# Optimization experiments

Hardware: AMD Instinct MI355X
Metric: run time of the kernel (lower is better)

The kernel has to match this reference:

```python
import jax, jax.numpy as jnp
import numpy as np

B, N, H, HD = 2, 2048, 16, 64
F = H * HD  # feats = 1024
SQRT_D = float(F) ** 0.5  # module uses sqrt(feats), not sqrt(head_dim)
EPS = 1e-5


def layernorm(x, g, b):
    # LayerNorm over last dim (head_dim), shared gamma/beta across heads
    m = jnp.mean(x, axis=-1, keepdims=True)
    v = jnp.mean(jnp.square(x - m), axis=-1, keepdims=True)
    return (x - m) / jnp.sqrt(v + EPS) * g + b


def setup_inputs() -> dict:
    key = jax.random.key(0)
    ks = jax.random.split(key, 14)
    s = 0.02
    return {
        "x": jax.random.normal(ks[0], (B, N, F), dtype=jnp.float32),
        "ln1_g": jnp.ones((HD,), jnp.float32),
        "ln1_b": jnp.zeros((HD,), jnp.float32),
        "ln2_g": jnp.ones((HD,), jnp.float32),
        "ln2_b": jnp.zeros((HD,), jnp.float32),
        # stacked per-head weights: [H, in, out]
        "wq": jax.random.normal(ks[1], (H, HD, HD), jnp.float32) * s,
        "bq": jnp.zeros((H, HD), jnp.float32),
        "wk": jax.random.normal(ks[2], (H, HD, HD), jnp.float32) * s,
        "bk": jnp.zeros((H, HD), jnp.float32),
        "wv": jax.random.normal(ks[3], (H, HD, HD), jnp.float32) * s,
        "bv": jnp.zeros((H, HD), jnp.float32),
        "wo": jax.random.normal(ks[4], (H, HD, HD), jnp.float32) * s,
        "bo": jnp.zeros((H, HD), jnp.float32),
        "w1": jax.random.normal(ks[5], (H, HD, 4 * HD), jnp.float32) * s,
        "b1": jnp.zeros((H, 4 * HD), jnp.float32),
        "w2": jax.random.normal(ks[6], (H, 4 * HD, HD), jnp.float32) * s,
        "b2": jnp.zeros((H, HD), jnp.float32),
        # Method 0 merge Linear(feats, feats): y = x @ wm + bm
        "wm": jax.random.normal(ks[7], (F, F), jnp.float32) * s,
        "bm": jnp.zeros((F,), jnp.float32),
    }


def reference(x, ln1_g, ln1_b, ln2_g, ln2_b, wq, bq, wk, bk, wv, bv, wo, bo,
              w1, b1, w2, b2, wm, bm):
    b, n, f = x.shape
    x4 = x.reshape(b, n, H, HD)  # [b, n, h, hd]

    # --- Multi-head self attention (per-head linears batched over h) ---
    h1 = layernorm(x4, ln1_g, ln1_b)
    q = jnp.einsum("bnhf,hfg->bnhg", h1, wq) + bq
    k = jnp.einsum("bnhf,hfg->bnhg", h1, wk) + bk
    v = jnp.einsum("bnhf,hfg->bnhg", h1, wv) + bv
    qh = jnp.swapaxes(q, 1, 2)  # [b, h, n, hd]
    kh = jnp.swapaxes(k, 1, 2)
    vh = jnp.swapaxes(v, 1, 2)
    score = jax.nn.softmax(jnp.einsum("bhif,bhjf->bhij", qh, kh) / SQRT_D, axis=-1)
    attn = jnp.einsum("bhij,bhjf->bihf", score, vh)  # [b, n, h, hd]
    attn = jnp.einsum("bnhf,hfg->bnhg", attn, wo) + bo
    out = attn + x4

    # --- Per-head FFN (GELU after BOTH linears, as in source; dropout=0) ---
    h2 = layernorm(out, ln2_g, ln2_b)
    t = jax.nn.gelu(jnp.einsum("bnhf,hfg->bnhg", h2, w1) + b1, approximate=False)
    t = jax.nn.gelu(jnp.einsum("bnhg,hgf->bnhf", t, w2) + b2, approximate=False)
    out = t + out

    # --- Method 0 merge ---
    out = out.reshape(b, n, f)
    out = out @ wm + bm
    return out
```

## Files before the change

kernel.cpp:

```cpp
#include <hip/hip_runtime.h>
#include <hip/hip_bf16.h>
#include <math.h>

#define TOKS 4096
#define NSEQ 2048
#define NH 16
#define DH 64
#define FD 1024

typedef __bf16 bf16_t;
typedef bf16_t bf16x4 __attribute__((ext_vector_type(4)));
typedef bf16_t bf16x8 __attribute__((ext_vector_type(8)));
typedef float f32x4 __attribute__((ext_vector_type(4)));

#define GLL16(gsrc, ldst)                                                        \
    __builtin_amdgcn_global_load_lds(                                            \
        (const __attribute__((address_space(1))) void*)(const void*)(gsrc),      \
        (__attribute__((address_space(3))) void*)(void*)(ldst), 16, 0, 0)

__device__ __forceinline__ float geluf(float x) {
    return 0.5f * x * (1.0f + erff(x * 0.70710678118654752f));
}

__device__ __forceinline__ int lds_sw(int row, int d) {
    return row * 64 + ((((d >> 3) ^ (row & 7)) & 7) << 3) + (d & 7);
}

__device__ __forceinline__ int vperm(int j) {
    return (j & 32) | ((j & 12) << 1) | ((j & 16) >> 2) | (j & 3);
}

__global__ __launch_bounds__(256) void k_prep(
    const float* __restrict__ wm, const float* __restrict__ w1, const float* __restrict__ w2,
    const float* __restrict__ wq, const float* __restrict__ wk,
    const float* __restrict__ wv, const float* __restrict__ wo,
    bf16_t* __restrict__ wt, bf16_t* __restrict__ w1t, bf16_t* __restrict__ w2t,
    bf16_t* __restrict__ wqt, bf16_t* __restrict__ wkt,
    bf16_t* __restrict__ wvt, bf16_t* __restrict__ wot)
{
    __shared__ bf16_t t[64 * 65];
    const int b = blockIdx.x;
    const int tid = threadIdx.x;
    if (b < 256) {
        const int k0 = (b & 15) * 64, n0 = (b >> 4) * 64;
        #pragma unroll
        for (int it = 0; it < 16; it++) {
            int idx = it * 256 + tid;
            int kk = idx >> 6, nn = idx & 63;
            t[nn * 65 + kk] = (bf16_t)wm[(size_t)(k0 + kk) * FD + n0 + nn];
        }
        __syncthreads();
        #pragma unroll
        for (int it = 0; it < 16; it++) {
            int idx = it * 256 + tid;
            int nn = idx >> 6, kk = idx & 63;
            wt[(size_t)(n0 + nn) * FD + k0 + kk] = t[nn * 65 + kk];
        }
    } else if (b < 320) {
        const int lb = b - 256;
        const int h = lb >> 2, n0 = (lb & 3) * 64;
        const float* src = w1 + (size_t)h * 64 * 256;
        #pragma unroll
        for (int it = 0; it < 16; it++) {
            int idx = it * 256 + tid;
            int kk = idx >> 6, nn = idx & 63;
            t[nn * 65 + kk] = (bf16_t)src[kk * 256 + n0 + nn];
        }
        __syncthreads();
        bf16_t* dst = w1t + (size_t)h * 16384;
        #pragma unroll
        for (int it = 0; it < 16; it++) {
            int idx = it * 256 + tid;
            int nn = idx >> 6, kk = idx & 63;
            int row = n0 + nn;
            dst[row * 64 + ((((kk >> 3) ^ (row & 7)) & 7) << 3) + (kk & 7)] = t[nn * 65 + kk];
        }
    } else if (b < 384) {
        const int lb = b - 320;
        const int h = lb >> 2, k0 = (lb & 3) * 64;
        const float* src = w2 + (size_t)h * 256 * 64;
        #pragma unroll
        for (int it = 0; it < 16; it++) {
            int idx = it * 256 + tid;
            int kk = idx >> 6, nn = idx & 63;
            t[nn * 65 + kk] = (bf16_t)src[(k0 + kk) * 64 + nn];
        }
        __syncthreads();
        bf16_t* dst = w2t + (size_t)h * 16384;
        #pragma unroll
        for (int it = 0; it < 16; it++) {
            int idx = it * 256 + tid;
            int nn = idx >> 6, kk = idx & 63;
            int c = k0 + vperm(kk);
            int chunk = c >> 3;
            int chunkp = (chunk & 24) | ((chunk ^ nn) & 7);
            dst[nn * 256 + (chunkp << 3) + (c & 7)] = t[nn * 65 + kk];
        }
    } else {
        const int h = b - 384;
        const float* srcs[4] = {wq + h * 4096, wk + h * 4096, wv + h * 4096, wo + h * 4096};
        bf16_t* dsts[4] = {wqt + h * 4096, wkt + h * 4096, wvt + h * 4096, wot + h * 4096};
        #pragma unroll
        for (int m = 0; m < 4; m++) {
            __syncthreads();
            #pragma unroll
            for (int it = 0; it < 16; it++) {
                int idx = it * 256 + tid;
                int ff = idx >> 6, gg = idx & 63;
                t[gg * 65 + ff] = (bf16_t)srcs[m][ff * 64 + gg];
            }
            __syncthreads();
            #pragma unroll
            for (int it = 0; it < 16; it++) {
                int idx = it * 256 + tid;
                int gg = idx >> 6, ff = idx & 63;
                if (m == 3)
                    dsts[m][gg * 64 + ((((ff >> 3) ^ (gg & 7)) & 7) << 3) + (ff & 7)] =
                        t[gg * 65 + ff];
                else
                    dsts[m][gg * 64 + ff] = t[gg * 65 + ff];
            }
        }
    }
}

__global__ __launch_bounds__(256) void k_ln1_qkv(
    const float* __restrict__ x, const float* __restrict__ g1, const float* __restrict__ be1,
    const bf16_t* __restrict__ wqt, const float* __restrict__ bq,
    const bf16_t* __restrict__ wkt, const float* __restrict__ bk,
    const bf16_t* __restrict__ wvt, const float* __restrict__ bv,
    bf16_t* __restrict__ q, bf16_t* __restrict__ k, bf16_t* __restrict__ vt)
{
    __shared__ __align__(16) bf16_t h1s[64 * 64];
    __shared__ __align__(16) bf16_t vts[64 * 72];
    const int h  = blockIdx.y;
    const int t0 = blockIdx.x * 64;
    const int tid = threadIdx.x;

    {
        const int i = tid >> 2, s = tid & 3;
        const float* xr = x + (size_t)(t0 + i) * FD + h * DH + s * 16;
        float vals[16];
        #pragma unroll
        for (int r = 0; r < 4; r++) {
            float4 tmp = *(const float4*)(xr + r * 4);
            vals[r*4+0]=tmp.x; vals[r*4+1]=tmp.y; vals[r*4+2]=tmp.z; vals[r*4+3]=tmp.w;
        }
        float sm = 0.f;
        #pragma unroll
        for (int r = 0; r < 16; r++) sm += vals[r];
        sm += __shfl_xor(sm, 1); sm += __shfl_xor(sm, 2);
        const float mean = sm * (1.0f / 64.0f);
        float vr = 0.f;
        #pragma unroll
        for (int r = 0; r < 16; r++) { float d = vals[r] - mean; vr += d * d; }
        vr += __shfl_xor(vr, 1); vr += __shfl_xor(vr, 2);
        const float rstd = rsqrtf(vr * (1.0f / 64.0f) + 1e-5f);
        bf16x8 o0, o1;
        #pragma unroll
        for (int r = 0; r < 8; r++) {
            int d0 = s * 16 + r, d1 = s * 16 + 8 + r;
            o0[r] = (bf16_t)((vals[r]     - mean) * rstd * g1[d0] + be1[d0]);
            o1[r] = (bf16_t)((vals[8 + r] - mean) * rstd * g1[d1] + be1[d1]);
        }
        *(bf16x8*)&h1s[i * 64 + (((s * 2 + 0) ^ (i & 7)) << 3)] = o0;
        *(bf16x8*)&h1s[i * 64 + (((s * 2 + 1) ^ (i & 7)) << 3)] = o1;
    }
    __syncthreads();

    const int wid = tid >> 6, lane = tid & 63;
    const int g = lane >> 4, c0 = lane & 15;
    const int arow = wid * 16 + c0;

    bf16x8 af0 = *(const bf16x8*)&h1s[arow * 64 + (((g    ) ^ (arow & 7)) << 3)];
    bf16x8 af1 = *(const bf16x8*)&h1s[arow * 64 + (((4 + g) ^ (arow & 7)) << 3)];

    const bf16_t* wqh = wqt + h * 4096;
    const bf16_t* wkh = wkt + h * 4096;
    const bf16_t* wvh = wvt + h * 4096;
    f32x4 aq[4], ak[4], av[4];
    #pragma unroll
    for (int ni = 0; ni < 4; ni++) {
        aq[ni] = (f32x4){0.f, 0.f, 0.f, 0.f};
        ak[ni] = (f32x4){0.f, 0.f, 0.f, 0.f};
        av[ni] = (f32x4){0.f, 0.f, 0.f, 0.f};
    }
    #pragma unroll
    for (int ni = 0; ni < 4; ni++) {
        const int col = ni * 16 + c0;
        bf16x8 b0, b1;
        b0 = *(const bf16x8*)(wqh + col * 64 + g * 8);
        b1 = *(const bf16x8*)(wqh + col * 64 + g * 8 + 32);
        aq[ni] = __builtin_amdgcn_mfma_f32_16x16x32_bf16(af0, b0, aq[ni], 0, 0, 0);
        aq[ni] = __builtin_amdgcn_mfma_f32_16x16x32_bf16(af1, b1, aq[ni], 0, 0, 0);
        b0 = *(const bf16x8*)(wkh + col * 64 + g * 8);
        b1 = *(const bf16x8*)(wkh + col * 64 + g * 8 + 32);
        ak[ni] = __builtin_amdgcn_mfma_f32_16x16x32_bf16(af0, b0, ak[ni], 0, 0, 0);
        ak[ni] = __builtin_amdgcn_mfma_f32_16x16x32_bf16(af1, b1, ak[ni], 0, 0, 0);
        b0 = *(const bf16x8*)(wvh + col * 64 + g * 8);
        b1 = *(const bf16x8*)(wvh + col * 64 + g * 8 + 32);
        av[ni] = __builtin_amdgcn_mfma_f32_16x16x32_bf16(af0, b0, av[ni], 0, 0, 0);
        av[ni] = __builtin_amdgcn_mfma_f32_16x16x32_bf16(af1, b1, av[ni], 0, 0, 0);
    }

    const int rowb = wid * 16 + g * 4;
    const int b = t0 >> 11, n0 = t0 & (NSEQ - 1);
    const size_t qkbase = ((size_t)(b * NH + h) * NSEQ + n0) * DH;

    #pragma unroll
    for (int ni = 0; ni < 4; ni++) {
        const int col = ni * 16 + c0;
        const float bb = bv[h * 64 + col];
        #pragma unroll
        for (int r = 0; r < 4; r++) {
            int i = rowb + r;
            vts[col * 72 + vperm(i)] = (bf16_t)(av[ni][r] + bb);
        }
    }
    __syncthreads();

    #pragma unroll
    for (int ni = 0; ni < 4; ni++) {
        const int col = ni * 16 + c0;
        const float bb = bq[h * 64 + col];
        #pragma unroll
        for (int r = 0; r < 4; r++)
            h1s[lds_sw(rowb + r, col)] = (bf16_t)((aq[ni][r] + bb) * 0.045084220f);
    }
    __syncthreads();
    {
        const int row = tid >> 2, cp = (tid & 3) * 2;
        *(bf16x8*)(q + qkbase + row * DH + cp * 8) =
            *(const bf16x8*)&h1s[row * 64 + ((cp ^ (row & 7)) << 3)];
        *(bf16x8*)(q + qkbase + row * DH + (cp + 1) * 8) =
            *(const bf16x8*)&h1s[row * 64 + (((cp + 1) ^ (row & 7)) << 3)];
        const int d = tid >> 2, c16 = tid & 3;
        size_t vbase = ((size_t)(b * NH + h) * DH + d) * NSEQ + n0 + c16 * 16;
        *(bf16x8*)(vt + vbase)     = *(const bf16x8*)&vts[d * 72 + c16 * 16];
        *(bf16x8*)(vt + vbase + 8) = *(const bf16x8*)&vts[d * 72 + c16 * 16 + 8];
    }
    __syncthreads();

    #pragma unroll
    for (int ni = 0; ni < 4; ni++) {
        const int col = ni * 16 + c0;
        const float bb = bk[h * 64 + col];
        #pragma unroll
        for (int r = 0; r < 4; r++)
            h1s[lds_sw(rowb + r, col)] = (bf16_t)(ak[ni][r] + bb);
    }
    __syncthreads();
    {
        const int row = tid >> 2, cp = (tid & 3) * 2;
        *(bf16x8*)(k + qkbase + row * DH + cp * 8) =
            *(const bf16x8*)&h1s[row * 64 + ((cp ^ (row & 7)) << 3)];
        *(bf16x8*)(k + qkbase + row * DH + (cp + 1) * 8) =
            *(const bf16x8*)&h1s[row * 64 + (((cp + 1) ^ (row & 7)) << 3)];
    }
}

__global__ __launch_bounds__(256, 4) void k_attn(
    const bf16_t* __restrict__ qg, const bf16_t* __restrict__ kg,
    const bf16_t* __restrict__ vt, bf16_t* __restrict__ attnb)
{
    __shared__ __align__(16) bf16_t Ks[2][4096];
    __shared__ __align__(16) bf16_t Vs[2][4096];

    const int bx = blockIdx.x;
    const int bh = ((bx & 7) << 2) | ((bx >> 3) & 3);
    const int qb = blockIdx.y;
    const int tid = threadIdx.x;
    const int wid = tid >> 6, lane = tid & 63;
    const int g = lane >> 4, c0 = lane & 15;
    const int prow = wid * 16 + c0;

    bf16x8 aqf[2];
    {
        const int qrow = qb * 64 + prow;
        const bf16_t* qp = qg + ((size_t)bh * NSEQ + qrow) * DH + g * 8;
        aqf[0] = *(const bf16x8*)qp;
        aqf[1] = *(const bf16x8*)(qp + 32);
    }
    bf16x8 ones;
    #pragma unroll
    for (int e = 0; e < 8; e++) ones[e] = (bf16_t)1.0f;

    int soff[4][2];
    #pragma unroll
    for (int cb = 0; cb < 4; cb++)
        #pragma unroll
        for (int kb = 0; kb < 2; kb++) {
            int row = cb * 16 + c0;
            soff[cb][kb] = row * 64 + (((g + (kb << 2)) ^ (row & 7)) << 3);
        }

    const bf16_t* kbase = kg + (size_t)bh * NSEQ * DH;
    const bf16_t* vbase = vt + (size_t)bh * DH * NSEQ;
    const int gA = wid * 2, gB = gA + 1;
    const int lcA = gA * 64 + lane, lcB = gB * 64 + lane;
    const int rowA = lcA >> 3, ccA = (lcA & 7) ^ (rowA & 7);
    const int rowB = lcB >> 3, ccB = (lcB & 7) ^ (rowB & 7);
    const bf16_t* kpA = kbase + rowA * DH + ccA * 8;
    const bf16_t* kpB = kbase + rowB * DH + ccB * 8;
    const bf16_t* vpA = vbase + (size_t)rowA * NSEQ + ccA * 8;
    const bf16_t* vpB = vbase + (size_t)rowB * NSEQ + ccB * 8;

    GLL16(kpA, (char*)&Ks[0][0] + (gA << 10));
    GLL16(kpB, (char*)&Ks[0][0] + (gB << 10));
    GLL16(vpA, (char*)&Vs[0][0] + (gA << 10));
    GLL16(vpB, (char*)&Vs[0][0] + (gB << 10));
    kpA += 64 * DH; kpB += 64 * DH; vpA += 64; vpB += 64;

    f32x4 O[4];
    #pragma unroll
    for (int cb = 0; cb < 4; cb++) O[cb] = (f32x4){0.f, 0.f, 0.f, 0.f};
    f32x4 l_acc = (f32x4){0.f, 0.f, 0.f, 0.f};

    auto tile = [&](const bf16_t* Kc, const bf16_t* Vc,
                    bf16_t* Kn, bf16_t* Vn, bool pref) {
        __syncthreads();
        if (pref) {
            GLL16(kpA, (char*)Kn + (gA << 10));
            GLL16(kpB, (char*)Kn + (gB << 10));
            GLL16(vpA, (char*)Vn + (gA << 10));
            GLL16(vpB, (char*)Vn + (gB << 10));
            kpA += 64 * DH; kpB += 64 * DH; vpA += 64; vpB += 64;
        }

        f32x4 S[4];
        #pragma unroll
        for (int cb = 0; cb < 4; cb++) {
            f32x4 acc = (f32x4){0.f, 0.f, 0.f, 0.f};
            acc = __builtin_amdgcn_mfma_f32_16x16x32_bf16(
                *(const bf16x8*)&Kc[soff[cb][0]], aqf[0], acc, 0, 0, 0);
            acc = __builtin_amdgcn_mfma_f32_16x16x32_bf16(
                *(const bf16x8*)&Kc[soff[cb][1]], aqf[1], acc, 0, 0, 0);
            S[cb] = acc;
        }

        bf16x8 pa0, pa1;
        #pragma unroll
        for (int cb = 0; cb < 2; cb++)
            #pragma unroll
            for (int r = 0; r < 4; r++)
                pa0[cb * 4 + r] = (bf16_t)exp2f(S[cb][r]);
        #pragma unroll
        for (int cb = 0; cb < 2; cb++)
            #pragma unroll
            for (int r = 0; r < 4; r++)
                pa1[cb * 4 + r] = (bf16_t)exp2f(S[2 + cb][r]);

        l_acc = __builtin_amdgcn_mfma_f32_16x16x32_bf16(ones, pa0, l_acc, 0, 0, 0);
        l_acc = __builtin_amdgcn_mfma_f32_16x16x32_bf16(ones, pa1, l_acc, 0, 0, 0);

        #pragma unroll
        for (int cb = 0; cb < 4; cb++) {
            f32x4 acc = O[cb];
            acc = __builtin_amdgcn_mfma_f32_16x16x32_bf16(
                *(const bf16x8*)&Vc[soff[cb][0]], pa0, acc, 0, 0, 0);
            acc = __builtin_amdgcn_mfma_f32_16x16x32_bf16(
                *(const bf16x8*)&Vc[soff[cb][1]], pa1, acc, 0, 0, 0);
            O[cb] = acc;
        }
    };

    #pragma unroll 1
    for (int kt2 = 0; kt2 < 16; kt2++) {
        tile(Ks[0], Vs[0], Ks[1], Vs[1], true);
        tile(Ks[1], Vs[1], Ks[0], Vs[0], kt2 < 15);
    }

    __syncthreads();
    const float inv = 1.0f / l_acc[0];
    bf16_t* Tb = Ks[0];
    #pragma unroll
    for (int cb = 0; cb < 4; cb++)
        #pragma unroll
        for (int r = 0; r < 4; r++) {
            int d = cb * 16 + g * 4 + r;
            Tb[lds_sw(prow, d)] = (bf16_t)(O[cb][r] * inv);
        }
    __syncthreads();
    {
        const int row = tid >> 2, cp = (tid & 3) * 2;
        size_t gbase = ((size_t)bh * NSEQ + qb * 64 + row) * DH;
        *(bf16x8*)(attnb + gbase + cp * 8) =
            *(const bf16x8*)&Tb[row * 64 + ((cp ^ (row & 7)) << 3)];
        *(bf16x8*)(attnb + gbase + (cp + 1) * 8) =
            *(const bf16x8*)&Tb[row * 64 + (((cp + 1) ^ (row & 7)) << 3)];
    }
}

__global__ __launch_bounds__(1024) void k_pffn(
    const bf16_t* __restrict__ attnb, const bf16_t* __restrict__ wot,
    const float* __restrict__ bo, const float* __restrict__ x,
    const float* __restrict__ g2, const float* __restrict__ be2,
    const bf16_t* __restrict__ w1t, const float* __restrict__ b1,
    const bf16_t* __restrict__ w2t, const float* __restrict__ b2,
    bf16_t* __restrict__ outp)
{
    __shared__ __align__(16) bf16_t wos[4096];
    __shared__ __align__(16) bf16_t w1s[16384];
    __shared__ __align__(16) bf16_t w2s[16384];
    __shared__ __align__(16) bf16_t h2s[256 * 64];
    const int h  = blockIdx.y;
    const int t0 = blockIdx.x * 256;
    const int tid = threadIdx.x;
    const int wid = tid >> 6, lane = tid & 63;
    const int g = lane >> 4, c0 = lane & 15;
    const int b = t0 >> 11, n0 = t0 & (NSEQ - 1);
    const int tok = t0 + wid * 16 + c0;

    {
        const bf16_t* s0 = wot + h * 4096;
        const bf16_t* s1 = w1t + (size_t)h * 16384;
        const bf16_t* s2 = w2t + (size_t)h * 16384;
        if (wid < 8)
            GLL16(s0 + wid * 512 + lane * 8, (char*)wos + (wid << 10));
        #pragma unroll
        for (int i = 0; i < 2; i++) {
            int grp = wid * 2 + i;
            GLL16(s1 + grp * 512 + lane * 8, (char*)w1s + (grp << 10));
            GLL16(s2 + grp * 512 + lane * 8, (char*)w2s + (grp << 10));
        }
        __syncthreads();
    }

    const bf16_t* ah = attnb + ((size_t)(b * NH + h) * NSEQ + n0) * DH;
    bf16x8 paf0 = *(const bf16x8*)(ah + (wid * 16 + c0) * DH + g * 8);
    bf16x8 paf1 = *(const bf16x8*)(ah + (wid * 16 + c0) * DH + g * 8 + 32);
    float o1[4][4];
    #pragma unroll
    for (int ni = 0; ni < 4; ni++) {
        f32x4 acc = (f32x4){0.f, 0.f, 0.f, 0.f};
        const int orow = ni * 16 + c0;
        bf16x8 b0  = *(const bf16x8*)&wos[orow * 64 + (((g    ) ^ (orow & 7)) << 3)];
        bf16x8 b1f = *(const bf16x8*)&wos[orow * 64 + (((4 + g) ^ (orow & 7)) << 3)];
        acc = __builtin_amdgcn_mfma_f32_16x16x32_bf16(b0, paf0, acc, 0, 0, 0);
        acc = __builtin_amdgcn_mfma_f32_16x16x32_bf16(b1f, paf1, acc, 0, 0, 0);
        const float4 bo4 = *(const float4*)(bo + h * DH + ni * 16 + g * 4);
        const float4 xr4 = *(const float4*)(x + (size_t)tok * FD + h * DH + ni * 16 + g * 4);
        o1[ni][0] = acc[0] + bo4.x + xr4.x;
        o1[ni][1] = acc[1] + bo4.y + xr4.y;
        o1[ni][2] = acc[2] + bo4.z + xr4.z;
        o1[ni][3] = acc[3] + bo4.w + xr4.w;
    }

    float s = 0.f;
    #pragma unroll
    for (int ni = 0; ni < 4; ni++)
        #pragma unroll
        for (int r = 0; r < 4; r++) s += o1[ni][r];
    s += __shfl_xor(s, 16);
    s += __shfl_xor(s, 32);
    const float mean = s * (1.0f / 64.0f);
    float v = 0.f;
    #pragma unroll
    for (int ni = 0; ni < 4; ni++)
        #pragma unroll
        for (int r = 0; r < 4; r++) { float d = o1[ni][r] - mean; v += d * d; }
    v += __shfl_xor(v, 16);
    v += __shfl_xor(v, 32);
    const float rstd = rsqrtf(v * (1.0f / 64.0f) + 1e-5f);

    const int R = wid * 16 + c0;
    #pragma unroll
    for (int ni = 0; ni < 4; ni++) {
        const float4 g24 = *(const float4*)(g2 + ni * 16 + g * 4);
        const float4 be4 = *(const float4*)(be2 + ni * 16 + g * 4);
        bf16x4 hw;
        hw[0] = (bf16_t)((o1[ni][0] - mean) * rstd * g24.x + be4.x);
        hw[1] = (bf16_t)((o1[ni][1] - mean) * rstd * g24.y + be4.y);
        hw[2] = (bf16_t)((o1[ni][2] - mean) * rstd * g24.z + be4.z);
        hw[3] = (bf16_t)((o1[ni][3] - mean) * rstd * g24.w + be4.w);
        int cc = ni * 2 + (g >> 1);
        *(bf16x4*)&h2s[R * 64 + ((cc ^ (R & 7)) << 3) + (g & 1) * 4] = hw;
    }
    bf16x8 af0 = *(const bf16x8*)&h2s[R * 64 + (((g    ) ^ (R & 7)) << 3)];
    bf16x8 af1 = *(const bf16x8*)&h2s[R * 64 + (((4 + g) ^ (R & 7)) << 3)];

    const float* b1h = b1 + h * 256;
    f32x4 acc2[4];
    #pragma unroll
    for (int nt = 0; nt < 4; nt++) acc2[nt] = (f32x4){0.f, 0.f, 0.f, 0.f};

    #pragma unroll
    for (int ub = 0; ub < 4; ub++) {
        f32x4 a4[4];
        #pragma unroll
        for (int j = 0; j < 4; j++) {
            const int wrow = (ub * 4 + j) * 16 + c0;
            bf16x8 bf0 = *(const bf16x8*)&w1s[wrow * 64 + (((g    ) ^ (wrow & 7)) << 3)];
            bf16x8 bf1 = *(const bf16x8*)&w1s[wrow * 64 + (((4 + g) ^ (wrow & 7)) << 3)];
            f32x4 acc = (f32x4){0.f, 0.f, 0.f, 0.f};
            acc = __builtin_amdgcn_mfma_f32_16x16x32_bf16(bf0, af0, acc, 0, 0, 0);
            acc = __builtin_amdgcn_mfma_f32_16x16x32_bf16(bf1, af1, acc, 0, 0, 0);
            a4[j] = acc;
        }
        float4 bb0 = *(const float4*)(b1h + (ub * 4 + 0) * 16 + g * 4);
        float4 bb1 = *(const float4*)(b1h + (ub * 4 + 1) * 16 + g * 4);
        float4 bb2 = *(const float4*)(b1h + (ub * 4 + 2) * 16 + g * 4);
        float4 bb3 = *(const float4*)(b1h + (ub * 4 + 3) * 16 + g * 4);
        bf16x8 p0, p1;
        #pragma unroll
        for (int r = 0; r < 4; r++) {
            p0[r]     = (bf16_t)geluf(a4[0][r] + ((const float*)&bb0)[r]);
            p0[4 + r] = (bf16_t)geluf(a4[1][r] + ((const float*)&bb1)[r]);
            p1[r]     = (bf16_t)geluf(a4[2][r] + ((const float*)&bb2)[r]);
            p1[4 + r] = (bf16_t)geluf(a4[3][r] + ((const float*)&bb3)[r]);
        }
        #pragma unroll
        for (int nt = 0; nt < 4; nt++) {
            const int vrow = nt * 16 + c0;
            bf16x8 bw0 = *(const bf16x8*)&w2s[vrow * 256 +
                            ((ub * 8 + ((g    ) ^ (vrow & 7))) << 3)];
            bf16x8 bw1 = *(const bf16x8*)&w2s[vrow * 256 +
                            ((ub * 8 + ((g + 4) ^ (vrow & 7))) << 3)];
            acc2[nt] = __builtin_amdgcn_mfma_f32_16x16x32_bf16(bw0, p0, acc2[nt], 0, 0, 0);
            acc2[nt] = __builtin_amdgcn_mfma_f32_16x16x32_bf16(bw1, p1, acc2[nt], 0, 0, 0);
        }
    }

    const float* b2h = b2 + h * 64;
    #pragma unroll
    for (int nt = 0; nt < 4; nt++) {
        const float4 b24 = *(const float4*)(b2h + nt * 16 + g * 4);
        bf16x4 ow;
        ow[0] = (bf16_t)(geluf(acc2[nt][0] + b24.x) + o1[nt][0]);
        ow[1] = (bf16_t)(geluf(acc2[nt][1] + b24.y) + o1[nt][1]);
        ow[2] = (bf16_t)(geluf(acc2[nt][2] + b24.z) + o1[nt][2]);
        ow[3] = (bf16_t)(geluf(acc2[nt][3] + b24.w) + o1[nt][3]);
        *(bf16x4*)(outp + (size_t)tok * FD + h * DH + nt * 16 + g * 4) = ow;
    }
}

__global__ __launch_bounds__(256) void k_merge(
    const bf16_t* __restrict__ A, const bf16_t* __restrict__ Wt, const float* __restrict__ bias,
    float* __restrict__ C)
{
    __shared__ __align__(16) bf16_t As[128 * 64];
    __shared__ __align__(16) bf16_t Bs[64 * 64];
    const int n0 = blockIdx.x * 64;
    const int m0 = blockIdx.y * 128;
    const int tid = threadIdx.x;
    const int wid = tid >> 6, lane = tid & 63;
    const int c0 = lane & 15, g = lane >> 4;

    const bf16_t* aS[4]; int aO[4];
    #pragma unroll
    for (int i = 0; i < 4; i++) {
        int grp = wid * 4 + i;
        int lc = grp * 64 + lane;
        int row = lc >> 3, cc = (lc & 7) ^ (row & 7);
        aS[i] = A + (size_t)(m0 + row) * FD + cc * 8;
        aO[i] = grp << 10;
    }
    const bf16_t* bS[2]; int bO[2];
    #pragma unroll
    for (int i = 0; i < 2; i++) {
        int grp = wid * 2 + i;
        int lc = grp * 64 + lane;
        int row = lc >> 3, cc = (lc & 7) ^ (row & 7);
        bS[i] = Wt + (size_t)(n0 + row) * FD + cc * 8;
        bO[i] = grp << 10;
    }

    f32x4 acc[2][4];
    #pragma unroll
    for (int mi = 0; mi < 2; mi++)
        #pragma unroll
        for (int ni = 0; ni < 4; ni++)
            acc[mi][ni] = (f32x4){0.f, 0.f, 0.f, 0.f};

    float bv[4];
    #pragma unroll
    for (int ni = 0; ni < 4; ni++) bv[ni] = bias[n0 + ni * 16 + c0];

    for (int k0 = 0; k0 < FD; k0 += 64) {
        __syncthreads();
        #pragma unroll
        for (int i = 0; i < 4; i++) GLL16(aS[i] + k0, (char*)As + aO[i]);
        #pragma unroll
        for (int i = 0; i < 2; i++) GLL16(bS[i] + k0, (char*)Bs + bO[i]);
        __syncthreads();

        bf16x8 af[2][2];
        #pragma unroll
        for (int mi = 0; mi < 2; mi++)
            #pragma unroll
            for (int kk = 0; kk < 2; kk++) {
                int arow = wid * 32 + mi * 16 + c0;
                int ch = kk * 4 + g;
                af[mi][kk] = *(const bf16x8*)&As[arow * 64 + ((ch ^ (arow & 7)) << 3)];
            }
        bf16x8 bfr[4][2];
        #pragma unroll
        for (int ni = 0; ni < 4; ni++)
            #pragma unroll
            for (int kk = 0; kk < 2; kk++) {
                int brow = ni * 16 + c0;
                int ch = kk * 4 + g;
                bfr[ni][kk] = *(const bf16x8*)&Bs[brow * 64 + ((ch ^ (brow & 7)) << 3)];
            }
        #pragma unroll
        for (int mi = 0; mi < 2; mi++)
            #pragma unroll
            for (int ni = 0; ni < 4; ni++)
                #pragma unroll
                for (int kk = 0; kk < 2; kk++)
                    acc[mi][ni] = __builtin_amdgcn_mfma_f32_16x16x32_bf16(
                        af[mi][kk], bfr[ni][kk], acc[mi][ni], 0, 0, 0);
    }

    #pragma unroll
    for (int mi = 0; mi < 2; mi++)
        #pragma unroll
        for (int r = 0; r < 4; r++) {
            int row = m0 + wid * 32 + mi * 16 + g * 4 + r;
            float* cp = C + (size_t)row * FD + n0;
            #pragma unroll
            for (int ni = 0; ni < 4; ni++)
                cp[ni * 16 + c0] = acc[mi][ni][r] + bv[ni];
        }
}

extern "C" void kernel_launch(void* const* d_in, const int* in_sizes, int n_in,
                              void* d_out, int out_size, void* d_ws, size_t ws_size,
                              hipStream_t stream) {
    const float* x   = (const float*)d_in[0];
    const float* g1  = (const float*)d_in[1];
    const float* be1 = (const float*)d_in[2];
    const float* g2  = (const float*)d_in[3];
    const float* be2 = (const float*)d_in[4];
    const float* wq  = (const float*)d_in[5];
    const float* bq  = (const float*)d_in[6];
    const float* wk  = (const float*)d_in[7];
    const float* bk  = (const float*)d_in[8];
    const float* wv  = (const float*)d_in[9];
    const float* bv  = (const float*)d_in[10];
    const float* wo  = (const float*)d_in[11];
    const float* bo  = (const float*)d_in[12];
    const float* w1  = (const float*)d_in[13];
    const float* b1  = (const float*)d_in[14];
    const float* w2  = (const float*)d_in[15];
    const float* b2  = (const float*)d_in[16];
    const float* wm  = (const float*)d_in[17];
    const float* bm  = (const float*)d_in[18];

    char* wsb = (char*)d_ws;
    bf16_t* qb_   = (bf16_t*)(wsb);
    bf16_t* kb_   = (bf16_t*)(wsb + (size_t)8  * 1048576);
    bf16_t* vtb   = (bf16_t*)(wsb + (size_t)16 * 1048576);
    bf16_t* attnb = (bf16_t*)(wsb + (size_t)24 * 1048576);
    bf16_t* out2  = (bf16_t*)(wsb + (size_t)40 * 1048576);
    bf16_t* wtb   = (bf16_t*)(wsb + (size_t)56 * 1048576);
    bf16_t* w1tb  = (bf16_t*)(wsb + (size_t)58 * 1048576);
    bf16_t* w2tb  = (bf16_t*)(wsb + (size_t)58 * 1048576 + 524288);
    bf16_t* wqtb  = (bf16_t*)(wsb + (size_t)59 * 1048576);
    bf16_t* wktb  = (bf16_t*)(wsb + (size_t)59 * 1048576 + 131072);
    bf16_t* wvtb  = (bf16_t*)(wsb + (size_t)59 * 1048576 + 262144);
    bf16_t* wotb  = (bf16_t*)(wsb + (size_t)59 * 1048576 + 393216);

    k_prep<<<dim3(400), 256, 0, stream>>>(wm, w1, w2, wq, wk, wv, wo,
                                          wtb, w1tb, w2tb, wqtb, wktb, wvtb, wotb);
    k_ln1_qkv<<<dim3(TOKS / 64, NH), 256, 0, stream>>>(x, g1, be1, wqtb, bq, wktb, bk, wvtb, bv,
                                                       qb_, kb_, vtb);
    k_attn<<<dim3(32, NSEQ / 64), 256, 0, stream>>>(qb_, kb_, vtb, attnb);
    k_pffn<<<dim3(TOKS / 256, NH), 1024, 0, stream>>>(attnb, wotb, bo, x, g2, be2,
                                                      w1tb, b1, w2tb, b2, out2);
    k_merge<<<dim3(FD / 64, TOKS / 128), 256, 0, stream>>>(out2, wtb, bm, (float*)d_out);
}
```

Baseline: 117.6 us.

## Process two query sub-tiles per wave in attention to reuse K/V tiles

```diff
diff --git a/kernel.cpp b/kernel.cpp
--- a/kernel.cpp
+++ b/kernel.cpp
@@ -259,7 +259,7 @@
     }
 }
 
-__global__ __launch_bounds__(256, 4) void k_attn(
+__global__ __launch_bounds__(256, 2) void k_attn(
     const bf16_t* __restrict__ qg, const bf16_t* __restrict__ kg,
     const bf16_t* __restrict__ vt, bf16_t* __restrict__ attnb)
 {
@@ -272,14 +272,14 @@
     const int tid = threadIdx.x;
     const int wid = tid >> 6, lane = tid & 63;
     const int g = lane >> 4, c0 = lane & 15;
-    const int prow = wid * 16 + c0;
-
-    bf16x8 aqf[2];
-    {
-        const int qrow = qb * 64 + prow;
+
+    bf16x8 aqf[2][2];
+    #pragma unroll
+    for (int m = 0; m < 2; m++) {
+        const int qrow = qb * 128 + wid * 32 + m * 16 + c0;
         const bf16_t* qp = qg + ((size_t)bh * NSEQ + qrow) * DH + g * 8;
-        aqf[0] = *(const bf16x8*)qp;
-        aqf[1] = *(const bf16x8*)(qp + 32);
+        aqf[m][0] = *(const bf16x8*)qp;
+        aqf[m][1] = *(const bf16x8*)(qp + 32);
     }
     bf16x8 ones;
     #pragma unroll
@@ -311,10 +311,14 @@
     GLL16(vpB, (char*)&Vs[0][0] + (gB << 10));
     kpA += 64 * DH; kpB += 64 * DH; vpA += 64; vpB += 64;
 
-    f32x4 O[4];
-    #pragma unroll
-    for (int cb = 0; cb < 4; cb++) O[cb] = (f32x4){0.f, 0.f, 0.f, 0.f};
-    f32x4 l_acc = (f32x4){0.f, 0.f, 0.f, 0.f};
+    f32x4 O[2][4];
+    #pragma unroll
+    for (int m = 0; m < 2; m++)
+        #pragma unroll
+        for (int cb = 0; cb < 4; cb++) O[m][cb] = (f32x4){0.f, 0.f, 0.f, 0.f};
+    f32x4 l_acc[2];
+    l_acc[0] = (f32x4){0.f, 0.f, 0.f, 0.f};
+    l_acc[1] = (f32x4){0.f, 0.f, 0.f, 0.f};
 
     auto tile = [&](const bf16_t* Kc, const bf16_t* Vc,
                     bf16_t* Kn, bf16_t* Vn, bool pref) {
@@ -327,41 +331,54 @@
             kpA += 64 * DH; kpB += 64 * DH; vpA += 64; vpB += 64;
         }
 
-        f32x4 S[4];
+        __builtin_amdgcn_s_setprio(1);
+        f32x4 S[2][4];
+        #pragma unroll
+        for (int m = 0; m < 2; m++)
+            #pragma unroll
+            for (int cb = 0; cb < 4; cb++) {
+                f32x4 acc = (f32x4){0.f, 0.f, 0.f, 0.f};
+                acc = __builtin_amdgcn_mfma_f32_16x16x32_bf16(
+                    *(const bf16x8*)&Kc[soff[cb][0]], aqf[m][0], acc, 0, 0, 0);
+                acc = __builtin_amdgcn_mfma_f32_16x16x32_bf16(
+                    *(const bf16x8*)&Kc[soff[cb][1]], aqf[m][1], acc, 0, 0, 0);
+                S[m][cb] = acc;
+            }
+
+        bf16x8 pa[2][2];
+        #pragma unroll
+        for (int m = 0; m < 2; m++) {
+            #pragma unroll
+            for (int cb = 0; cb < 2; cb++)
+                #pragma unroll
+                for (int r = 0; r < 4; r++)
+                    pa[m][0][cb * 4 + r] = (bf16_t)exp2f(S[m][cb][r]);
+            #pragma unroll
+            for (int cb = 0; cb < 2; cb++)
+                #pragma unroll
+                for (int r = 0; r < 4; r++)
+                    pa[m][1][cb * 4 + r] = (bf16_t)exp2f(S[m][2 + cb][r]);
+        }
+
+        #pragma unroll
+        for (int m = 0; m < 2; m++) {
+            l_acc[m] = __builtin_amdgcn_mfma_f32_16x16x32_bf16(ones, pa[m][0], l_acc[m], 0, 0, 0);
+            l_acc[m] = __builtin_amdgcn_mfma_f32_16x16x32_bf16(ones, pa[m][1], l_acc[m], 0, 0, 0);
+        }
+
         #pragma unroll
         for (int cb = 0; cb < 4; cb++) {
-            f32x4 acc = (f32x4){0.f, 0.f, 0.f, 0.f};
-            acc = __builtin_amdgcn_mfma_f32_16x16x32_bf16(
-                *(const bf16x8*)&Kc[soff[cb][0]], aqf[0], acc, 0, 0, 0);
-            acc = __builtin_amdgcn_mfma_f32_16x16x32_bf16(
-                *(const bf16x8*)&Kc[soff[cb][1]], aqf[1], acc, 0, 0, 0);
-            S[cb] = acc;
-        }
-
-        bf16x8 pa0, pa1;
-        #pragma unroll
-        for (int cb = 0; cb < 2; cb++)
-            #pragma unroll
-            for (int r = 0; r < 4; r++)
-                pa0[cb * 4 + r] = (bf16_t)exp2f(S[cb][r]);
-        #pragma unroll
-        for (int cb = 0; cb < 2; cb++)
-            #pragma unroll
-            for (int r = 0; r < 4; r++)
-                pa1[cb * 4 + r] = (bf16_t)exp2f(S[2 + cb][r]);
-
-        l_acc = __builtin_amdgcn_mfma_f32_16x16x32_bf16(ones, pa0, l_acc, 0, 0, 0);
-        l_acc = __builtin_amdgcn_mfma_f32_16x16x32_bf16(ones, pa1, l_acc, 0, 0, 0);
-
-        #pragma unroll
-        for (int cb = 0; cb < 4; cb++) {
-            f32x4 acc = O[cb];
-            acc = __builtin_amdgcn_mfma_f32_16x16x32_bf16(
-                *(const bf16x8*)&Vc[soff[cb][0]], pa0, acc, 0, 0, 0);
-            acc = __builtin_amdgcn_mfma_f32_16x16x32_bf16(
-                *(const bf16x8*)&Vc[soff[cb][1]], pa1, acc, 0, 0, 0);
-            O[cb] = acc;
-        }
+            bf16x8 vb0 = *(const bf16x8*)&Vc[soff[cb][0]];
+            bf16x8 vb1 = *(const bf16x8*)&Vc[soff[cb][1]];
+            #pragma unroll
+            for (int m = 0; m < 2; m++) {
+                f32x4 acc = O[m][cb];
+                acc = __builtin_amdgcn_mfma_f32_16x16x32_bf16(vb0, pa[m][0], acc, 0, 0, 0);
+                acc = __builtin_amdgcn_mfma_f32_16x16x32_bf16(vb1, pa[m][1], acc, 0, 0, 0);
+                O[m][cb] = acc;
+            }
+        }
+        __builtin_amdgcn_s_setprio(0);
     };
 
     #pragma unroll 1
@@ -370,20 +387,27 @@
         tile(Ks[1], Vs[1], Ks[0], Vs[0], kt2 < 15);
     }
 
-    __syncthreads();
-    const float inv = 1.0f / l_acc[0];
     bf16_t* Tb = Ks[0];
     #pragma unroll
-    for (int cb = 0; cb < 4; cb++)
-        #pragma unroll
-        for (int r = 0; r < 4; r++) {
-            int d = cb * 16 + g * 4 + r;
-            Tb[lds_sw(prow, d)] = (bf16_t)(O[cb][r] * inv);
-        }
-    __syncthreads();
-    {
+    for (int p = 0; p < 2; p++) {
+        __syncthreads();
+        if ((wid >> 1) == p) {
+            #pragma unroll
+            for (int m = 0; m < 2; m++) {
+                const float inv = 1.0f / l_acc[m][0];
+                const int lrow = (wid & 1) * 32 + m * 16 + c0;
+                #pragma unroll
+                for (int cb = 0; cb < 4; cb++)
+                    #pragma unroll
+                    for (int r = 0; r < 4; r++) {
+                        int d = cb * 16 + g * 4 + r;
+                        Tb[lds_sw(lrow, d)] = (bf16_t)(O[m][cb][r] * inv);
+                    }
+            }
+        }
+        __syncthreads();
         const int row = tid >> 2, cp = (tid & 3) * 2;
-        size_t gbase = ((size_t)bh * NSEQ + qb * 64 + row) * DH;
+        size_t gbase = ((size_t)bh * NSEQ + qb * 128 + p * 64 + row) * DH;
         *(bf16x8*)(attnb + gbase + cp * 8) =
             *(const bf16x8*)&Tb[row * 64 + ((cp ^ (row & 7)) << 3)];
         *(bf16x8*)(attnb + gbase + (cp + 1) * 8) =
@@ -665,7 +689,7 @@
                                           wtb, w1tb, w2tb, wqtb, wktb, wvtb, wotb);
     k_ln1_qkv<<<dim3(TOKS / 64, NH), 256, 0, stream>>>(x, g1, be1, wqtb, bq, wktb, bk, wvtb, bv,
                                                        qb_, kb_, vtb);
-    k_attn<<<dim3(32, NSEQ / 64), 256, 0, stream>>>(qb_, kb_, vtb, attnb);
+    k_attn<<<dim3(32, NSEQ / 128), 256, 0, stream>>>(qb_, kb_, vtb, attnb);
     k_pffn<<<dim3(TOKS / 256, NH), 1024, 0, stream>>>(attnb, wotb, bo, x, g2, be2,
                                                       w1tb, b1, w2tb, b2, out2);
     k_merge<<<dim3(FD / 64, TOKS / 128), 256, 0, stream>>>(out2, wtb, bm, (float*)d_out);
```

Result: no change. 117.3 us (-0.3%).
